# Kernel tuning notes

Hardware: AMD Instinct MI355X
Metric: run time of the kernel (lower is better)

The kernel has to match this reference:

```python
import jax, jax.numpy as jnp
import numpy as np

IN_FEATURES = 1024
OUT_FEATURES = 1024
GRID_SIZE = 5
SPLINE_ORDER = 3
GRID_RANGE = (-1.0, 1.0)


def make_grid():
    h = (GRID_RANGE[1] - GRID_RANGE[0]) / GRID_SIZE
    knots = jnp.arange(-SPLINE_ORDER, GRID_SIZE + SPLINE_ORDER + 1, dtype=jnp.float32) * h + GRID_RANGE[0]
    return jnp.broadcast_to(knots, (IN_FEATURES, knots.shape[0]))  # (in, 12)


def b_splines(x, knots, p):
    # x: (B, in); knots: (in, nk). Cox-de Boor recursion, degree p.
    xs = x[:, :, None]                                   # (B, in, 1)
    bases = ((xs >= knots[None, :, :-1]) & (xs < knots[None, :, 1:])).astype(x.dtype)
    for k in range(1, p + 1):
        den1 = knots[:, k:-1] - knots[:, :-(k + 1)]
        den1 = jnp.where(den1 == 0, jnp.float32(1e-8), den1)
        den2 = knots[:, k + 1:] - knots[:, 1:-k]
        den2 = jnp.where(den2 == 0, jnp.float32(1e-8), den2)
        term1 = (xs - knots[None, :, :-(k + 1)]) / den1[None] * bases[:, :, :-1]
        term2 = (knots[None, :, k + 1:] - xs) / den2[None] * bases[:, :, 1:]
        bases = term1 + term2
    return bases  # (B, in, grid_size + p)


def setup_inputs() -> dict:
    key = jax.random.key(0)
    k1, k2, k3, k4 = jax.random.split(key, 4)
    K = GRID_SIZE + SPLINE_ORDER
    x = jax.random.normal(k1, (4096, IN_FEATURES), dtype=jnp.float32)
    base_weight = jax.random.normal(k2, (OUT_FEATURES, IN_FEATURES), dtype=jnp.float32) * (1.0 / np.sqrt(IN_FEATURES))
    spline_weight = jax.random.normal(k3, (OUT_FEATURES, IN_FEATURES, K), dtype=jnp.float32) * 0.02
    spline_scaler = jax.random.normal(k4, (OUT_FEATURES, IN_FEATURES), dtype=jnp.float32) * (1.0 / np.sqrt(IN_FEATURES))
    grid = make_grid()
    return {"x": x, "base_weight": base_weight, "spline_weight": spline_weight,
            "spline_scaler": spline_scaler, "grid": grid}


def reference(x, base_weight, spline_weight, spline_scaler, grid):
    base_out = jax.nn.silu(x) @ base_weight.T                      # (B, out)
    bases = b_splines(x, grid, SPLINE_ORDER)                       # (B, in, K)
    scaled_sw = spline_weight * spline_scaler[:, :, None]          # (out, in, K)
    spline_out = jnp.einsum('bik,oik->bo', bases, scaled_sw)       # (B, out)
    return base_out + spline_out
```

## Files before the change

kernel.cpp:

```cpp
#include <hip/hip_runtime.h>
#include <hip/hip_bf16.h>
#include <cstdint>
#include <cstddef>

#define AS1 __attribute__((address_space(1)))
#define AS3 __attribute__((address_space(3)))

typedef __bf16 bf16;
typedef __bf16 bf16x8 __attribute__((ext_vector_type(8)));
typedef float f32x4 __attribute__((ext_vector_type(4)));

static constexpr int M_ROWS = 4096;
static constexpr int N_COLS = 1024;
static constexpr int IN_F   = 1024;
static constexpr int K2     = IN_F * 9;
static constexpr int BK     = 32;
static constexpr int KT_CNT = K2 / BK;

static constexpr int GBK = 64;
static constexpr int GKT = K2 / GBK;


__device__ __forceinline__ void bases8(float x, float w8[8]) {
  float mf = x * 2.5f + 5.5f;
  int   m  = (int)floorf(mf);
  float u  = mf - (float)m;
  float u2 = u * u, u3 = u2 * u;
  float omu = 1.0f - u;
  const float s = 1.0f / 6.0f;
  float p0 = u3 * s;
  float p1 = (-3.f*u3 + 3.f*u2 + 3.f*u + 1.f) * s;
  float p2 = (3.f*u3 - 6.f*u2 + 4.f) * s;
  float p3 = omu * omu * omu * s;
  bool in = (m >= 0) && (m < 11);
#pragma unroll
  for (int j = 0; j < 8; ++j) {
    float v = 0.0f;
    v = (j == m)     ? p0 : v;
    v = (j == m - 1) ? p1 : v;
    v = (j == m - 2) ? p2 : v;
    v = (j == m - 3) ? p3 : v;
    w8[j] = in ? v : 0.0f;
  }
}

__global__ void expand_a(const float* __restrict__ x, bf16* __restrict__ A,
                         int r0) {
  int gid = blockIdx.x * blockDim.x + threadIdx.x;
  int b = gid >> 10;
  int i = gid & 1023;
  float xv = x[(size_t)r0 * IN_F + (size_t)gid];

  A[(size_t)b * K2 + i] = (bf16)(xv / (1.0f + __expf(-xv)));

  float w8[8];
  bases8(xv, w8);
  bf16x8 outv;
#pragma unroll
  for (int j = 0; j < 8; ++j) outv[j] = (bf16)w8[j];
  *(bf16x8*)(A + (size_t)b * K2 + IN_F + (size_t)i * 8) = outv;
}

__global__ void make_bt(const float* __restrict__ bw, const float* __restrict__ sw,
                        const float* __restrict__ sc, bf16* __restrict__ BT) {
  int gid = blockIdx.x * blockDim.x + threadIdx.x;
  int o = gid >> 10;
  int i = gid & 1023;

  BT[(size_t)o * K2 + i] = (bf16)bw[gid];

  float scale = sc[gid];
  const float4* swp = (const float4*)(sw + (size_t)gid * 8);
  float4 a = swp[0], b4 = swp[1];
  float wv[8] = {a.x, a.y, a.z, a.w, b4.x, b4.y, b4.z, b4.w};
  bf16x8 r;
#pragma unroll
  for (int j = 0; j < 8; ++j) r[j] = (bf16)(wv[j] * scale);
  *(bf16x8*)(BT + (size_t)o * K2 + IN_F + (size_t)i * 8) = r;
}

__global__ __launch_bounds__(512, 1) void gemm256(
    const bf16* __restrict__ A, const bf16* __restrict__ BT,
    float* __restrict__ P, int kt_seg) {
  __shared__ bf16 As[2][256 * GBK];
  __shared__ bf16 Bs[2][256 * GBK];

  const int tid  = threadIdx.x;
  const int lane = tid & 63;
  const int w    = tid >> 6;

  const int b     = blockIdx.x;
  const int mtile = b & 15;
  const int np    = (b >> 4) & 3;
  const int seg   = b >> 6;
  const int row0  = mtile * 256;
  const int col0  = np * 256;
  const int kt0   = seg * kt_seg;
  float* __restrict__ dst = P + (size_t)seg * M_ROWS * N_COLS;

  const int srow = lane >> 3;
  const int sch  = ((lane & 7) ^ srow) * 8;

  const int r  = lane & 15;
  const int q  = lane >> 4;
  const int wm = (w >> 2) * 128;
  const int wn = (w & 3) * 64;
  const int kc0 = ((0 + q) ^ (r & 7)) * 8;
  const int kc1 = ((4 + q) ^ (r & 7)) * 8;

  const bf16* aB = A  + (size_t)row0 * K2;
  const bf16* bB = BT + (size_t)col0 * K2;

  f32x4 acc[8][4];
#pragma unroll
  for (int mt = 0; mt < 8; ++mt)
#pragma unroll
    for (int nt = 0; nt < 4; ++nt)
      acc[mt][nt] = f32x4{0.f, 0.f, 0.f, 0.f};

  auto stage = [&](int sbuf, int kt) {
#pragma unroll
    for (int t = 0; t < 4; ++t) {
      const int rg = w * 32 + t * 8;
      const bf16* ga = aB + (size_t)(rg + srow) * K2 + kt * GBK + sch;
      __builtin_amdgcn_global_load_lds((const AS1 void*)ga,
                                       (AS3 void*)&As[sbuf][rg * GBK], 16, 0, 0);
      const bf16* gb = bB + (size_t)(rg + srow) * K2 + kt * GBK + sch;
      __builtin_amdgcn_global_load_lds((const AS1 void*)gb,
                                       (AS3 void*)&Bs[sbuf][rg * GBK], 16, 0, 0);
    }
  };

  stage(0, kt0);
  int buf = 0;
  for (int i = 0; i < kt_seg; ++i) {
    if (i + 1 < kt_seg) {
      stage(buf ^ 1, kt0 + i + 1);
      asm volatile("s_waitcnt vmcnt(8)" ::: "memory");
    } else {
      asm volatile("s_waitcnt vmcnt(0)" ::: "memory");
    }
    __builtin_amdgcn_s_barrier();
    __builtin_amdgcn_sched_barrier(0);

    const bf16* as = As[buf];
    const bf16* bs = Bs[buf];

#pragma unroll
    for (int kk = 0; kk < 2; ++kk) {
      const int kc = kk ? kc1 : kc0;
      bf16x8 af[8], bfr[4];
#pragma unroll
      for (int mt = 0; mt < 8; ++mt)
        af[mt] = *(const bf16x8*)&as[(wm + mt * 16 + r) * GBK + kc];
#pragma unroll
      for (int nt = 0; nt < 4; ++nt)
        bfr[nt] = *(const bf16x8*)&bs[(wn + nt * 16 + r) * GBK + kc];
      __builtin_amdgcn_s_setprio(1);
#pragma unroll
      for (int mt = 0; mt < 8; ++mt)
#pragma unroll
        for (int nt = 0; nt < 4; ++nt)
          acc[mt][nt] = __builtin_amdgcn_mfma_f32_16x16x32_bf16(
              af[mt], bfr[nt], acc[mt][nt], 0, 0, 0);
      __builtin_amdgcn_s_setprio(0);
    }
    __builtin_amdgcn_s_barrier();
    buf ^= 1;
  }

#pragma unroll
  for (int mt = 0; mt < 8; ++mt)
#pragma unroll
    for (int nt = 0; nt < 4; ++nt)
#pragma unroll
      for (int k = 0; k < 4; ++k) {
        int row = row0 + wm + mt * 16 + q * 4 + k;
        int col = col0 + wn + nt * 16 + r;
        dst[(size_t)row * N_COLS + col] = acc[mt][nt][k];
      }
}

__global__ __launch_bounds__(256, 2) void gemm_fused(
    const bf16* __restrict__ A, const bf16* __restrict__ BT,
    float* __restrict__ d0, float* __restrict__ d1,
    int r0, int mt_cnt, int kt_seg) {
  __shared__ bf16 As[2][128 * GBK];
  __shared__ bf16 Bs[2][128 * GBK];

  const int tid  = threadIdx.x;
  const int lane = tid & 63;
  const int w    = tid >> 6;

  const int bps = mt_cnt * 8;
  int b   = blockIdx.x;
  const int seg = b / bps;
  b -= seg * bps;
  const int row0 = (b % mt_cnt) * 128;
  const int col0 = (b / mt_cnt) * 128;
  float* __restrict__ dst = seg ? d1 : d0;
  const int kt0 = seg * kt_seg;

  const int srow = lane >> 3;
  const int sch  = ((lane & 7) ^ srow) * 8;
  const int r  = lane & 15;
  const int q  = lane >> 4;
  const int wm = (w >> 1) * 64;
  const int wn = (w & 1) * 64;
  const int kc0 = ((0 + q) ^ (r & 7)) * 8;
  const int kc1 = ((4 + q) ^ (r & 7)) * 8;

  const bf16* aB = A  + (size_t)row0 * K2;
  const bf16* bB = BT + (size_t)col0 * K2;

  f32x4 acc[4][4];
#pragma unroll
  for (int mt = 0; mt < 4; ++mt)
#pragma unroll
    for (int nt = 0; nt < 4; ++nt)
      acc[mt][nt] = f32x4{0.f, 0.f, 0.f, 0.f};

  auto stage = [&](int sbuf, int kt) {
#pragma unroll
    for (int t = 0; t < 4; ++t) {
      const int rg = w * 32 + t * 8;
      const bf16* ga = aB + (size_t)(rg + srow) * K2 + kt * GBK + sch;
      __builtin_amdgcn_global_load_lds((const AS1 void*)ga,
                                       (AS3 void*)&As[sbuf][rg * GBK], 16, 0, 0);
      const bf16* gb = bB + (size_t)(rg + srow) * K2 + kt * GBK + sch;
      __builtin_amdgcn_global_load_lds((const AS1 void*)gb,
                                       (AS3 void*)&Bs[sbuf][rg * GBK], 16, 0, 0);
    }
  };

  stage(0, kt0);
  int buf = 0;
  for (int i = 0; i < kt_seg; ++i) {
    if (i + 1 < kt_seg) {
      stage(buf ^ 1, kt0 + i + 1);
      asm volatile("s_waitcnt vmcnt(8)" ::: "memory");
    } else {
      asm volatile("s_waitcnt vmcnt(0)" ::: "memory");
    }
    __builtin_amdgcn_s_barrier();
    __builtin_amdgcn_sched_barrier(0);

    const bf16* as = As[buf];
    const bf16* bs = Bs[buf];

#pragma unroll
    for (int kk = 0; kk < 2; ++kk) {
      const int kc = kk ? kc1 : kc0;
      bf16x8 af[4], bfr[4];
#pragma unroll
      for (int mt = 0; mt < 4; ++mt)
        af[mt] = *(const bf16x8*)&as[(wm + mt * 16 + r) * GBK + kc];
#pragma unroll
      for (int nt = 0; nt < 4; ++nt)
        bfr[nt] = *(const bf16x8*)&bs[(wn + nt * 16 + r) * GBK + kc];
#pragma unroll
      for (int mt = 0; mt < 4; ++mt)
#pragma unroll
        for (int nt = 0; nt < 4; ++nt)
          acc[mt][nt] = __builtin_amdgcn_mfma_f32_16x16x32_bf16(
              af[mt], bfr[nt], acc[mt][nt], 0, 0, 0);
    }
    __builtin_amdgcn_s_barrier();
    buf ^= 1;
  }

#pragma unroll
  for (int mt = 0; mt < 4; ++mt)
#pragma unroll
    for (int nt = 0; nt < 4; ++nt)
#pragma unroll
      for (int k = 0; k < 4; ++k) {
        int row = r0 + row0 + wm + mt * 16 + q * 4 + k;
        int col = col0 + wn + nt * 16 + r;
        dst[(size_t)row * N_COLS + col] = acc[mt][nt][k];
      }
}

__global__ void reduce_addN(const float* __restrict__ P,
                            float* __restrict__ out, int segs) {
  size_t i = (size_t)blockIdx.x * blockDim.x + threadIdx.x;
  const f32x4* p = (const f32x4*)P;
  const size_t plane = (size_t)M_ROWS * N_COLS / 4;
  f32x4 a = p[i];
  for (int s = 1; s < segs; ++s) a += p[(size_t)s * plane + i];
  ((f32x4*)out)[i] = a;
}

__global__ __launch_bounds__(256) void kan_fused_fallback(
    const float* __restrict__ x, const float* __restrict__ bw,
    const float* __restrict__ sw, const float* __restrict__ sc,
    float* __restrict__ out) {
  __shared__ bf16 As[64 * BK];
  __shared__ bf16 Bs[128 * BK];
  const int tid  = threadIdx.x;
  const int lane = tid & 63;
  const int w    = tid >> 6;
  const int col0 = blockIdx.x * 128;
  const int row0 = blockIdx.y * 64;
  const int srow = tid >> 2, sq = tid & 3;
  const int r = lane & 15, q = lane >> 4, wn = w * 32;

  f32x4 acc[4][2];
#pragma unroll
  for (int mt = 0; mt < 4; ++mt)
#pragma unroll
    for (int nt = 0; nt < 2; ++nt) acc[mt][nt] = f32x4{0,0,0,0};

  for (int kt = 0; kt < KT_CNT; ++kt) {
    if (kt < 32) {
      const int cc = sq * 8;
      const float4* xp = (const float4*)(x + (size_t)(row0+srow)*IN_F + kt*BK + cc);
      float4 a = xp[0], b4 = xp[1];
      float xv[8] = {a.x,a.y,a.z,a.w,b4.x,b4.y,b4.z,b4.w};
      bf16x8 av;
#pragma unroll
      for (int j = 0; j < 8; ++j) av[j] = (bf16)(xv[j] / (1.0f + __expf(-xv[j])));
      *(bf16x8*)&As[srow * BK + cc] = av;
#pragma unroll
      for (int h = 0; h < 2; ++h) {
        const float4* bp = (const float4*)(bw + (size_t)(col0+h*64+srow)*IN_F + kt*BK + cc);
        float4 c0 = bp[0], c1 = bp[1];
        float bv[8] = {c0.x,c0.y,c0.z,c0.w,c1.x,c1.y,c1.z,c1.w};
        bf16x8 bb;
#pragma unroll
        for (int j = 0; j < 8; ++j) bb[j] = (bf16)bv[j];
        *(bf16x8*)&Bs[(h*64+srow)*BK + cc] = bb;
      }
    } else {
      const int i = (kt - 32) * 4 + sq;
      float xv = x[(size_t)(row0+srow)*IN_F + i];
      float w8[8]; bases8(xv, w8);
      bf16x8 av;
#pragma unroll
      for (int j = 0; j < 8; ++j) av[j] = (bf16)w8[j];
      *(bf16x8*)&As[srow * BK + sq * 8] = av;
#pragma unroll
      for (int h = 0; h < 2; ++h) {
        const int o = col0 + h*64 + srow;
        float s1 = sc[(size_t)o*IN_F + i];
        const float4* sp = (const float4*)(sw + ((size_t)o*IN_F + i)*8);
        float4 c0 = sp[0], c1 = sp[1];
        float wv[8] = {c0.x,c0.y,c0.z,c0.w,c1.x,c1.y,c1.z,c1.w};
        bf16x8 bb;
#pragma unroll
        for (int j = 0; j < 8; ++j) bb[j] = (bf16)(wv[j]*s1);
        *(bf16x8*)&Bs[(h*64+srow)*BK + sq*8] = bb;
      }
    }
    __syncthreads();
    bf16x8 af[4], bfr[2];
#pragma unroll
    for (int mt = 0; mt < 4; ++mt)
      af[mt] = *(const bf16x8*)&As[(mt*16+r)*BK + q*8];
#pragma unroll
    for (int nt = 0; nt < 2; ++nt)
      bfr[nt] = *(const bf16x8*)&Bs[(wn+nt*16+r)*BK + q*8];
#pragma unroll
    for (int mt = 0; mt < 4; ++mt)
#pragma unroll
      for (int nt = 0; nt < 2; ++nt)
        acc[mt][nt] = __builtin_amdgcn_mfma_f32_16x16x32_bf16(af[mt], bfr[nt], acc[mt][nt], 0,0,0);
    __syncthreads();
  }
#pragma unroll
  for (int mt = 0; mt < 4; ++mt)
#pragma unroll
    for (int nt = 0; nt < 2; ++nt)
#pragma unroll
      for (int k = 0; k < 4; ++k)
        out[(size_t)(row0+mt*16+q*4+k)*N_COLS + col0+wn+nt*16+r] = acc[mt][nt][k];
}

extern "C" void kernel_launch(void* const* d_in, const int* in_sizes, int n_in,
                              void* d_out, int out_size, void* d_ws, size_t ws_size,
                              hipStream_t stream) {
  const float* x    = (const float*)d_in[0];
  const float* bw   = (const float*)d_in[1];
  const float* sw   = (const float*)d_in[2];
  const float* sc   = (const float*)d_in[3];
  float* out = (float*)d_out;

  const size_t BT_BYTES  = (size_t)N_COLS * K2 * sizeof(bf16);
  const size_t ROW_BYTES = (size_t)K2 * sizeof(bf16);
  const size_t A_BYTES   = (size_t)M_ROWS * ROW_BYTES;
  const size_t OUT_BYTES = (size_t)M_ROWS * N_COLS * sizeof(float);

  int S = 0;
  for (int c = 4; c >= 2; --c)
    if (GKT % c == 0 && BT_BYTES + A_BYTES + (size_t)c * OUT_BYTES <= ws_size) {
      S = c; break;
    }

  if (S >= 2) {
    bf16*  BT    = (bf16*)d_ws;
    bf16*  Aslab = BT + (size_t)N_COLS * K2;
    float* P     = (float*)((char*)d_ws + BT_BYTES + A_BYTES);
    make_bt<<<(N_COLS * IN_F) / 256, 256, 0, stream>>>(bw, sw, sc, BT);
    expand_a<<<(M_ROWS * IN_F) / 256, 256, 0, stream>>>(x, Aslab, 0);
    gemm256<<<S * 64, 512, 0, stream>>>(Aslab, BT, P, GKT / S);
    reduce_addN<<<(M_ROWS * N_COLS) / (4 * 256), 256, 0, stream>>>(P, out, S);
  } else {
    int SL = 0;
    for (int cand = 4096; cand >= 128; cand >>= 1)
      if (BT_BYTES + (size_t)cand * ROW_BYTES <= ws_size) { SL = cand; break; }
    if (SL) {
      bf16* BT    = (bf16*)d_ws;
      bf16* Aslab = BT + (size_t)N_COLS * K2;
      make_bt<<<(N_COLS * IN_F) / 256, 256, 0, stream>>>(bw, sw, sc, BT);
      for (int r0 = 0; r0 < M_ROWS; r0 += SL) {
        expand_a<<<(SL * IN_F) / 256, 256, 0, stream>>>(x, Aslab, r0);
        gemm_fused<<<(SL / 128) * (N_COLS / 128), 256, 0, stream>>>(
            Aslab, BT, out, out, r0, SL / 128, GKT);
      }
    } else {
      kan_fused_fallback<<<dim3(N_COLS / 128, M_ROWS / 64), 256, 0, stream>>>(
          x, bw, sw, sc, out);
    }
  }
  (void)in_sizes; (void)n_in; (void)out_size;
}
```

Baseline: 208.2 us.

## Merge prep kernels and restructure GEMM main loop into interleaved 8-phase pipeline

Combines the A-expansion and BT-construction kernels into a single prep launch, which removes one kernel launch and lets both run concurrently. The 256x256 GEMM main loop is rewritten as an 8-phase schedule: each quarter of the warp tile's MFMAs is interleaved with LDS fragment reads and half-tile global-to-LDS prefetches, with finer-grained barriers and waitcnts. Launch bounds change to allow 2 blocks per CU. This aims to hide load latency behind matrix math, but it adds many more barriers, and two 512-thread blocks per CU may not fit given the 128 KB of LDS per block and the register demand.

```diff
diff --git a/kernel.cpp b/kernel.cpp
--- a/kernel.cpp
+++ b/kernel.cpp
@@ -44,15 +44,12 @@
   }
 }
 
-__global__ void expand_a(const float* __restrict__ x, bf16* __restrict__ A,
-                         int r0) {
-  int gid = blockIdx.x * blockDim.x + threadIdx.x;
+__device__ __forceinline__ void expand_body(const float* __restrict__ x,
+                                            bf16* __restrict__ A, int gid, int r0) {
   int b = gid >> 10;
   int i = gid & 1023;
   float xv = x[(size_t)r0 * IN_F + (size_t)gid];
-
   A[(size_t)b * K2 + i] = (bf16)(xv / (1.0f + __expf(-xv)));
-
   float w8[8];
   bases8(xv, w8);
   bf16x8 outv;
@@ -61,14 +58,13 @@
   *(bf16x8*)(A + (size_t)b * K2 + IN_F + (size_t)i * 8) = outv;
 }
 
-__global__ void make_bt(const float* __restrict__ bw, const float* __restrict__ sw,
-                        const float* __restrict__ sc, bf16* __restrict__ BT) {
-  int gid = blockIdx.x * blockDim.x + threadIdx.x;
+__device__ __forceinline__ void makebt_body(const float* __restrict__ bw,
+                                            const float* __restrict__ sw,
+                                            const float* __restrict__ sc,
+                                            bf16* __restrict__ BT, int gid) {
   int o = gid >> 10;
   int i = gid & 1023;
-
   BT[(size_t)o * K2 + i] = (bf16)bw[gid];
-
   float scale = sc[gid];
   const float4* swp = (const float4*)(sw + (size_t)gid * 8);
   float4 a = swp[0], b4 = swp[1];
@@ -79,7 +75,26 @@
   *(bf16x8*)(BT + (size_t)o * K2 + IN_F + (size_t)i * 8) = r;
 }
 
-__global__ __launch_bounds__(512, 1) void gemm256(
+__global__ void prep(const float* __restrict__ x, const float* __restrict__ bw,
+                     const float* __restrict__ sw, const float* __restrict__ sc,
+                     bf16* __restrict__ A, bf16* __restrict__ BT) {
+  int bid = blockIdx.x;
+  if (bid < (M_ROWS * IN_F) / 256) {
+    expand_body(x, A, bid * 256 + threadIdx.x, 0);
+  } else {
+    makebt_body(bw, sw, sc, BT, (bid - (M_ROWS * IN_F) / 256) * 256 + threadIdx.x);
+  }
+}
+
+__global__ void expand_a(const float* __restrict__ x, bf16* __restrict__ A, int r0) {
+  expand_body(x, A, blockIdx.x * blockDim.x + threadIdx.x, r0);
+}
+__global__ void make_bt(const float* __restrict__ bw, const float* __restrict__ sw,
+                        const float* __restrict__ sc, bf16* __restrict__ BT) {
+  makebt_body(bw, sw, sc, BT, blockIdx.x * blockDim.x + threadIdx.x);
+}
+
+__global__ __launch_bounds__(512, 2) void gemm256_8p(
     const bf16* __restrict__ A, const bf16* __restrict__ BT,
     float* __restrict__ P, int kt_seg) {
   __shared__ bf16 As[2][256 * GBK];
@@ -118,55 +133,126 @@
     for (int nt = 0; nt < 4; ++nt)
       acc[mt][nt] = f32x4{0.f, 0.f, 0.f, 0.f};
 
-  auto stage = [&](int sbuf, int kt) {
-#pragma unroll
-    for (int t = 0; t < 4; ++t) {
-      const int rg = w * 32 + t * 8;
+  auto stageA = [&](int sbuf, int h, int kt) {
+#pragma unroll
+    for (int t8 = 0; t8 < 2; ++t8) {
+      const int rg = h * 128 + w * 16 + t8 * 8;
       const bf16* ga = aB + (size_t)(rg + srow) * K2 + kt * GBK + sch;
       __builtin_amdgcn_global_load_lds((const AS1 void*)ga,
                                        (AS3 void*)&As[sbuf][rg * GBK], 16, 0, 0);
+    }
+  };
+  auto stageB = [&](int sbuf, int h, int kt) {
+#pragma unroll
+    for (int t8 = 0; t8 < 2; ++t8) {
+      const int rg = h * 128 + w * 16 + t8 * 8;
       const bf16* gb = bB + (size_t)(rg + srow) * K2 + kt * GBK + sch;
       __builtin_amdgcn_global_load_lds((const AS1 void*)gb,
                                        (AS3 void*)&Bs[sbuf][rg * GBK], 16, 0, 0);
     }
   };
 
-  stage(0, kt0);
-  int buf = 0;
-  for (int i = 0; i < kt_seg; ++i) {
-    if (i + 1 < kt_seg) {
-      stage(buf ^ 1, kt0 + i + 1);
-      asm volatile("s_waitcnt vmcnt(8)" ::: "memory");
-    } else {
-      asm volatile("s_waitcnt vmcnt(0)" ::: "memory");
-    }
-    __builtin_amdgcn_s_barrier();
-    __builtin_amdgcn_sched_barrier(0);
-
+  stageA(0, 0, kt0); stageA(0, 1, kt0);
+  stageB(0, 0, kt0); stageB(0, 1, kt0);
+  if (kt_seg > 1) stageA(1, 0, kt0 + 1);
+  if (kt_seg > 1) asm volatile("s_waitcnt vmcnt(2)" ::: "memory");
+  else            asm volatile("s_waitcnt vmcnt(0)" ::: "memory");
+  __builtin_amdgcn_s_barrier();
+
+  bf16x8 af[4][2], bfr[4][2];
+
+  for (int t = 0; t < kt_seg; ++t) {
+    const int buf = t & 1, nbuf = buf ^ 1;
     const bf16* as = As[buf];
     const bf16* bs = Bs[buf];
-
-#pragma unroll
-    for (int kk = 0; kk < 2; ++kk) {
-      const int kc = kk ? kc1 : kc0;
-      bf16x8 af[8], bfr[4];
-#pragma unroll
-      for (int mt = 0; mt < 8; ++mt)
-        af[mt] = *(const bf16x8*)&as[(wm + mt * 16 + r) * GBK + kc];
-#pragma unroll
-      for (int nt = 0; nt < 4; ++nt)
-        bfr[nt] = *(const bf16x8*)&bs[(wn + nt * 16 + r) * GBK + kc];
-      __builtin_amdgcn_s_setprio(1);
-#pragma unroll
-      for (int mt = 0; mt < 8; ++mt)
-#pragma unroll
-        for (int nt = 0; nt < 4; ++nt)
-          acc[mt][nt] = __builtin_amdgcn_mfma_f32_16x16x32_bf16(
-              af[mt], bfr[nt], acc[mt][nt], 0, 0, 0);
-      __builtin_amdgcn_s_setprio(0);
-    }
-    __builtin_amdgcn_s_barrier();
-    buf ^= 1;
+    const bool sN = (t + 1 < kt_seg);
+
+#pragma unroll
+    for (int j = 0; j < 4; ++j) {
+      const bf16* ar = &as[(wm + j * 16 + r) * GBK];
+      af[j][0] = *(const bf16x8*)&ar[kc0];
+      af[j][1] = *(const bf16x8*)&ar[kc1];
+    }
+#pragma unroll
+    for (int j = 0; j < 2; ++j) {
+      const bf16* br = &bs[(wn + j * 16 + r) * GBK];
+      bfr[j][0] = *(const bf16x8*)&br[kc0];
+      bfr[j][1] = *(const bf16x8*)&br[kc1];
+    }
+    if (sN) stageA(nbuf, 1, kt0 + t + 1);
+    asm volatile("s_waitcnt lgkmcnt(8)" ::: "memory");
+    __builtin_amdgcn_s_barrier();
+    asm volatile("s_waitcnt lgkmcnt(0)" ::: "memory");
+    __builtin_amdgcn_sched_barrier(0);
+    __builtin_amdgcn_s_setprio(1);
+#pragma unroll
+    for (int j = 0; j < 4; ++j)
+#pragma unroll
+      for (int n = 0; n < 2; ++n) {
+        acc[j][n] = __builtin_amdgcn_mfma_f32_16x16x32_bf16(af[j][0], bfr[n][0], acc[j][n], 0, 0, 0);
+        acc[j][n] = __builtin_amdgcn_mfma_f32_16x16x32_bf16(af[j][1], bfr[n][1], acc[j][n], 0, 0, 0);
+      }
+    __builtin_amdgcn_s_setprio(0);
+    __builtin_amdgcn_s_barrier();
+
+#pragma unroll
+    for (int j = 0; j < 2; ++j) {
+      const bf16* br = &bs[(wn + (2 + j) * 16 + r) * GBK];
+      bfr[2 + j][0] = *(const bf16x8*)&br[kc0];
+      bfr[2 + j][1] = *(const bf16x8*)&br[kc1];
+    }
+    if (sN) stageB(nbuf, 0, kt0 + t + 1);
+    __builtin_amdgcn_s_barrier();
+    asm volatile("s_waitcnt lgkmcnt(0)" ::: "memory");
+    __builtin_amdgcn_sched_barrier(0);
+    __builtin_amdgcn_s_setprio(1);
+#pragma unroll
+    for (int j = 0; j < 4; ++j)
+#pragma unroll
+      for (int n = 0; n < 2; ++n) {
+        acc[j][2 + n] = __builtin_amdgcn_mfma_f32_16x16x32_bf16(af[j][0], bfr[2 + n][0], acc[j][2 + n], 0, 0, 0);
+        acc[j][2 + n] = __builtin_amdgcn_mfma_f32_16x16x32_bf16(af[j][1], bfr[2 + n][1], acc[j][2 + n], 0, 0, 0);
+      }
+    __builtin_amdgcn_s_setprio(0);
+    __builtin_amdgcn_s_barrier();
+
+#pragma unroll
+    for (int j = 0; j < 4; ++j) {
+      const bf16* ar = &as[(wm + (4 + j) * 16 + r) * GBK];
+      af[j][0] = *(const bf16x8*)&ar[kc0];
+      af[j][1] = *(const bf16x8*)&ar[kc1];
+    }
+    if (sN) stageB(nbuf, 1, kt0 + t + 1);
+    __builtin_amdgcn_s_barrier();
+    asm volatile("s_waitcnt lgkmcnt(0)" ::: "memory");
+    __builtin_amdgcn_sched_barrier(0);
+    __builtin_amdgcn_s_setprio(1);
+#pragma unroll
+    for (int j = 0; j < 4; ++j)
+#pragma unroll
+      for (int n = 0; n < 2; ++n) {
+        acc[4 + j][n] = __builtin_amdgcn_mfma_f32_16x16x32_bf16(af[j][0], bfr[n][0], acc[4 + j][n], 0, 0, 0);
+        acc[4 + j][n] = __builtin_amdgcn_mfma_f32_16x16x32_bf16(af[j][1], bfr[n][1], acc[4 + j][n], 0, 0, 0);
+      }
+    __builtin_amdgcn_s_setprio(0);
+    __builtin_amdgcn_s_barrier();
+
+    if (t + 2 < kt_seg) stageA(buf, 0, kt0 + t + 2);
+    if (sN) {
+      if (t + 2 < kt_seg) asm volatile("s_waitcnt vmcnt(2)" ::: "memory");
+      else                asm volatile("s_waitcnt vmcnt(0)" ::: "memory");
+    }
+    __builtin_amdgcn_s_barrier();
+    __builtin_amdgcn_s_setprio(1);
+#pragma unroll
+    for (int j = 0; j < 4; ++j)
+#pragma unroll
+      for (int n = 0; n < 2; ++n) {
+        acc[4 + j][2 + n] = __builtin_amdgcn_mfma_f32_16x16x32_bf16(af[j][0], bfr[2 + n][0], acc[4 + j][2 + n], 0, 0, 0);
+        acc[4 + j][2 + n] = __builtin_amdgcn_mfma_f32_16x16x32_bf16(af[j][1], bfr[2 + n][1], acc[4 + j][2 + n], 0, 0, 0);
+      }
+    __builtin_amdgcn_s_setprio(0);
+    __builtin_amdgcn_s_barrier();
   }
 
 #pragma unroll
@@ -400,9 +486,9 @@
     bf16*  BT    = (bf16*)d_ws;
     bf16*  Aslab = BT + (size_t)N_COLS * K2;
     float* P     = (float*)((char*)d_ws + BT_BYTES + A_BYTES);
-    make_bt<<<(N_COLS * IN_F) / 256, 256, 0, stream>>>(bw, sw, sc, BT);
-    expand_a<<<(M_ROWS * IN_F) / 256, 256, 0, stream>>>(x, Aslab, 0);
-    gemm256<<<S * 64, 512, 0, stream>>>(Aslab, BT, P, GKT / S);
+    prep<<<(M_ROWS * IN_F) / 256 + (N_COLS * IN_F) / 256, 256, 0, stream>>>(
+        x, bw, sw, sc, Aslab, BT);
+    gemm256_8p<<<S * 64, 512, 0, stream>>>(Aslab, BT, P, GKT / S);
     reduce_addN<<<(M_ROWS * N_COLS) / (4 * 256), 256, 0, stream>>>(P, out, S);
   } else {
     int SL = 0;
```

Result: faster. 201.2 us (-3.3%).
